# Kernel optimization log

Measured on AMD Instinct MI355X. Metric: run time of the kernel, lower is better.

The kernel has to match this reference:

```python
import jax, jax.numpy as jnp
import numpy as np

NUM_HEADS = 32
NUM_KV_HEADS = 8
HEAD_DIM = 128


def setup_inputs() -> dict:
    key = jax.random.key(0)
    ks = jax.random.split(key, 5)
    B, S, H = 2, 2048, 4096
    Dq = NUM_HEADS * HEAD_DIM      # 4096
    Dkv = NUM_KV_HEADS * HEAD_DIM  # 1024
    return {
        "hidden_states": jax.random.normal(ks[0], (B, S, H), jnp.float32),
        "w_q": jax.random.normal(ks[1], (H, Dq), jnp.float32) * 0.02,
        "w_k": jax.random.normal(ks[2], (H, Dkv), jnp.float32) * 0.02,
        "w_v": jax.random.normal(ks[3], (H, Dkv), jnp.float32) * 0.02,
        "w_o": jax.random.normal(ks[4], (Dq, H), jnp.float32) * 0.02,
    }


def reference(hidden_states, w_q, w_k, w_v, w_o):
    # GQA causal attention, prefill path (no KV cache, RoPE is a no-op in source).
    B, S, _ = hidden_states.shape
    Hq, Hkv, D = NUM_HEADS, NUM_KV_HEADS, HEAD_DIM
    g = Hq // Hkv  # kv groups
    scale = D ** -0.5

    q = (hidden_states @ w_q).reshape(B, S, Hkv, g, D)  # [B,S,Hkv,g,D]
    k = (hidden_states @ w_k).reshape(B, S, Hkv, D)     # [B,S,Hkv,D]
    v = (hidden_states @ w_v).reshape(B, S, Hkv, D)

    # repeat_kv expressed as grouped einsum (avoids materializing repeated K/V)
    scores = jnp.einsum('bqhgd,bkhd->bhgqk', q, k) * scale  # [B,Hkv,g,S,S]
    causal = jnp.tril(jnp.ones((S, S), dtype=bool))
    scores = jnp.where(causal, scores, -jnp.inf)
    probs = jax.nn.softmax(scores.astype(jnp.float32), axis=-1).astype(q.dtype)

    attn = jnp.einsum('bhgqk,bkhd->bqhgd', probs, v)  # [B,S,Hkv,g,D]
    attn = attn.reshape(B, S, Hq * D)
    return attn @ w_o
```

## Files before the change

### kernel.cpp

```cpp
#include <hip/hip_runtime.h>

typedef unsigned short u16;
typedef __attribute__((ext_vector_type(8))) short bf16x8;
typedef __attribute__((ext_vector_type(8))) unsigned short u16x8;
typedef __attribute__((ext_vector_type(4))) unsigned short u16x4;
typedef __attribute__((ext_vector_type(4))) float f32x4;

__device__ __forceinline__ u16 f2bf(float f) {
  union { float f; unsigned u; } v; v.f = f;
  unsigned r = v.u + 0x7fffu + ((v.u >> 16) & 1u);
  return (u16)(r >> 16);
}

__device__ __forceinline__ void gload16(const u16* g, u16* l) {
  __builtin_amdgcn_global_load_lds((const __attribute__((address_space(1))) void*)g,
                                   (__attribute__((address_space(3))) void*)l, 16, 0, 0);
}

__device__ __forceinline__ void transpose_body(const float* __restrict__ in,
                                               u16* __restrict__ out, int K, int N,
                                               int bid, float (*tile)[65]) {
  int nbx = N >> 6;
  int n0 = (bid % nbx) << 6;
  int k0 = (bid / nbx) << 6;
  int tx = threadIdx.x & 15;
  int ty = threadIdx.x >> 4;
#pragma unroll
  for (int r = 0; r < 64; r += 16) {
    float4 v = *(const float4*)(in + (size_t)(k0 + ty + r) * N + n0 + tx * 4);
    tile[ty + r][tx * 4 + 0] = v.x;
    tile[ty + r][tx * 4 + 1] = v.y;
    tile[ty + r][tx * 4 + 2] = v.z;
    tile[ty + r][tx * 4 + 3] = v.w;
  }
  __syncthreads();
#pragma unroll
  for (int r = 0; r < 64; r += 16) {
    u16x4 o;
#pragma unroll
    for (int j = 0; j < 4; j++) o[j] = f2bf(tile[tx * 4 + j][ty + r]);
    *(u16x4*)(out + (size_t)(n0 + ty + r) * K + k0 + tx * 4) = o;
  }
}

__global__ __launch_bounds__(256) void prep_kern(const float* __restrict__ hs,
                                                 const float* __restrict__ wq,
                                                 const float* __restrict__ wk,
                                                 const float* __restrict__ wv,
                                                 const float* __restrict__ wo,
                                                 u16* __restrict__ hs_b,
                                                 u16* __restrict__ wqT,
                                                 u16* __restrict__ wkT,
                                                 u16* __restrict__ wvT,
                                                 u16* __restrict__ woT) {
  __shared__ float tile[64][65];
  int b = blockIdx.x;
  if (b < 8192) {
    int i = (b * 256 + threadIdx.x) * 8;
    float4 a = *(const float4*)(hs + i);
    float4 c = *(const float4*)(hs + i + 4);
    u16x8 r;
    r[0] = f2bf(a.x); r[1] = f2bf(a.y); r[2] = f2bf(a.z); r[3] = f2bf(a.w);
    r[4] = f2bf(c.x); r[5] = f2bf(c.y); r[6] = f2bf(c.z); r[7] = f2bf(c.w);
    *(u16x8*)(hs_b + i) = r;
  } else if (b < 12288) {
    transpose_body(wq, wqT, 4096, 4096, b - 8192, tile);
  } else if (b < 13312) {
    transpose_body(wk, wkT, 4096, 1024, b - 12288, tile);
  } else if (b < 14336) {
    transpose_body(wv, wvT, 4096, 1024, b - 13312, tile);
  } else {
    transpose_body(wo, woT, 4096, 4096, b - 14336, tile);
  }
}

#define PH_PRE()                                           \
  asm volatile("" ::: "memory");                           \
  __builtin_amdgcn_s_barrier();                            \
  asm volatile("" ::: "memory");                           \
  __builtin_amdgcn_s_setprio(1)

#define PH_POST()                                          \
  __builtin_amdgcn_s_setprio(0);                           \
  asm volatile("" ::: "memory");                           \
  __builtin_amdgcn_s_barrier();                            \
  asm volatile("" ::: "memory")

template <int MODE>
__global__ __launch_bounds__(512, 2) void gemm256(const u16* __restrict__ A,
                                                  const u16* __restrict__ Bt,
                                                  void* __restrict__ Cout,
                                                  int M, int N, int K) {
  __shared__ u16 lds[65536];
  const int tid = threadIdx.x;
  const int lane = tid & 63, w = tid >> 6;
  const int wm = w >> 2, wn = w & 3;
  const int li = lane & 15, lg = lane >> 4;
  const int NT = K >> 6;

  const int nbx = N >> 8;
  const int nwg = gridDim.x;
  const int swz = (blockIdx.x & 7) * (nwg >> 3) + (blockIdx.x >> 3);
  const int m0 = (swz / nbx) << 8;
  const int n0 = (swz % nbx) << 8;

  const int srow = w * 16 + (lane >> 3);
  const int scol = ((lane & 7) ^ (lane >> 3)) << 3;
  const u16* sA0 = A + (size_t)(m0 + srow) * K + scol;
  const u16* sA1 = A + (size_t)(m0 + 128 + srow) * K + scol;
  const u16* sB0 = Bt + (size_t)(n0 + srow) * K + scol;
  const u16* sB1 = Bt + (size_t)(n0 + 128 + srow) * K + scol;
  const size_t jK = (size_t)8 * K;
  u16* dA0 = lds + w * 1024;
  u16* dA1 = lds + 8192 + w * 1024;
  u16* dB0 = lds + 32768 + w * 1024;
  u16* dB1 = lds + 32768 + 8192 + w * 1024;

#define STG(sp, dp, t_) do {                                          \
    int db_ = (t_) & 1;                                               \
    gload16((sp) + (size_t)(t_) * 64, (dp) + db_ * 16384);            \
    gload16((sp) + (size_t)(t_) * 64 + jK, (dp) + db_ * 16384 + 512); \
  } while (0)

  STG(sA0, dA0, 0); STG(sA1, dA1, 0); STG(sB0, dB0, 0); STG(sB1, dB1, 0);
  STG(sA0, dA0, 1); STG(sA1, dA1, 1); STG(sB0, dB0, 1); STG(sB1, dB1, 1);
  asm volatile("s_waitcnt vmcnt(8)" ::: "memory");
  __builtin_amdgcn_s_barrier();
  asm volatile("" ::: "memory");

  f32x4 acc[8][4];
#pragma unroll
  for (int m = 0; m < 8; m++)
#pragma unroll
    for (int n = 0; n < 4; n++) acc[m][n] = (f32x4){0.f, 0.f, 0.f, 0.f};

  const int xsw = (li & 7) << 3;
  const int k0o = (lg * 8) ^ xsw;
  const int k1o = (32 + lg * 8) ^ xsw;
  const u16* aBase = lds + wm * 8192;
  const u16* bBase = lds + 32768 + (wn >> 1) * 8192;
  const int brow0 = (wn & 1) * 64;

  bf16x8 a[4][2], b[4][2];

  for (int t = 0; t < NT; ++t) {
    const int db = t & 1;
    const u16* Ab = aBase + db * 16384;
    const u16* Bb = bBase + db * 16384;

#pragma unroll
    for (int mf = 0; mf < 4; mf++) {
      int r = mf * 16 + li;
      a[mf][0] = *(const bf16x8*)(Ab + r * 64 + k0o);
      a[mf][1] = *(const bf16x8*)(Ab + r * 64 + k1o);
    }
#pragma unroll
    for (int nf = 0; nf < 2; nf++) {
      int r = brow0 + nf * 16 + li;
      b[nf][0] = *(const bf16x8*)(Bb + r * 64 + k0o);
      b[nf][1] = *(const bf16x8*)(Bb + r * 64 + k1o);
    }
    PH_PRE();
#pragma unroll
    for (int mf = 0; mf < 4; mf++)
#pragma unroll
      for (int nf = 0; nf < 2; nf++) {
        acc[mf][nf] = __builtin_amdgcn_mfma_f32_16x16x32_bf16(a[mf][0], b[nf][0], acc[mf][nf], 0, 0, 0);
        acc[mf][nf] = __builtin_amdgcn_mfma_f32_16x16x32_bf16(a[mf][1], b[nf][1], acc[mf][nf], 0, 0, 0);
      }
    PH_POST();

#pragma unroll
    for (int nf = 2; nf < 4; nf++) {
      int r = brow0 + nf * 16 + li;
      b[nf][0] = *(const bf16x8*)(Bb + r * 64 + k0o);
      b[nf][1] = *(const bf16x8*)(Bb + r * 64 + k1o);
    }
    PH_PRE();
#pragma unroll
    for (int mf = 0; mf < 4; mf++)
#pragma unroll
      for (int nf = 2; nf < 4; nf++) {
        acc[mf][nf] = __builtin_amdgcn_mfma_f32_16x16x32_bf16(a[mf][0], b[nf][0], acc[mf][nf], 0, 0, 0);
        acc[mf][nf] = __builtin_amdgcn_mfma_f32_16x16x32_bf16(a[mf][1], b[nf][1], acc[mf][nf], 0, 0, 0);
      }
    PH_POST();

#pragma unroll
    for (int mf = 0; mf < 4; mf++) {
      int r = (mf + 4) * 16 + li;
      a[mf][0] = *(const bf16x8*)(Ab + r * 64 + k0o);
      a[mf][1] = *(const bf16x8*)(Ab + r * 64 + k1o);
    }
    if (t + 2 < NT) { STG(sB0, dB0, t + 2); STG(sB1, dB1, t + 2); }
    PH_PRE();
#pragma unroll
    for (int mf = 0; mf < 4; mf++)
#pragma unroll
      for (int nf = 2; nf < 4; nf++) {
        acc[mf + 4][nf] = __builtin_amdgcn_mfma_f32_16x16x32_bf16(a[mf][0], b[nf][0], acc[mf + 4][nf], 0, 0, 0);
        acc[mf + 4][nf] = __builtin_amdgcn_mfma_f32_16x16x32_bf16(a[mf][1], b[nf][1], acc[mf + 4][nf], 0, 0, 0);
      }
    PH_POST();

    if (t + 2 < NT) { STG(sA0, dA0, t + 2); STG(sA1, dA1, t + 2); }
    PH_PRE();
#pragma unroll
    for (int mf = 0; mf < 4; mf++)
#pragma unroll
      for (int nf = 0; nf < 2; nf++) {
        acc[mf + 4][nf] = __builtin_amdgcn_mfma_f32_16x16x32_bf16(a[mf][0], b[nf][0], acc[mf + 4][nf], 0, 0, 0);
        acc[mf + 4][nf] = __builtin_amdgcn_mfma_f32_16x16x32_bf16(a[mf][1], b[nf][1], acc[mf + 4][nf], 0, 0, 0);
      }
    __builtin_amdgcn_s_setprio(0);
    if (t < NT - 2) {
      asm volatile("s_waitcnt vmcnt(8)" ::: "memory");
    } else {
      asm volatile("s_waitcnt vmcnt(0)" ::: "memory");
    }
    __builtin_amdgcn_s_barrier();
    asm volatile("" ::: "memory");
  }

#pragma unroll
  for (int mf = 0; mf < 8; mf++)
#pragma unroll
    for (int nf = 0; nf < 4; nf++)
#pragma unroll
      for (int r = 0; r < 4; r++) {
        int gm = m0 + wm * 128 + mf * 16 + lg * 4 + r;
        int gn = n0 + wn * 64 + nf * 16 + li;
        if (MODE == 0)
          ((u16*)Cout)[(size_t)gm * N + gn] = f2bf(acc[mf][nf][r]);
        else
          ((float*)Cout)[(size_t)gm * N + gn] = acc[mf][nf][r];
      }
#undef STG
}

__global__ __launch_bounds__(512, 2) void gemm_kv(const u16* __restrict__ A,
                                                  const u16* __restrict__ Bt,
                                                  u16* __restrict__ Kout,
                                                  u16* __restrict__ Vout) {
  __shared__ u16 lds[49152];
  const int tid = threadIdx.x;
  const int lane = tid & 63, w = tid >> 6;
  const int wm = w >> 2, wn = w & 3;
  const int li = lane & 15, lg = lane >> 4;
  const int K = 4096, NT = 64;

  const int swz = (blockIdx.x & 7) * 32 + (blockIdx.x >> 3);
  const int m0 = (swz >> 3) << 7;
  const int n0 = (swz & 7) << 8;

  const int srow = w * 16 + (lane >> 3);
  const int scol = ((lane & 7) ^ (lane >> 3)) << 3;
  const u16* sA  = A  + (size_t)(m0 + srow) * K + scol;
  const u16* sB0 = Bt + (size_t)(n0 + srow) * K + scol;
  const u16* sB1 = Bt + (size_t)(n0 + 128 + srow) * K + scol;
  const size_t jK = (size_t)8 * K;
  u16* dA  = lds + w * 1024;
  u16* dB0 = lds + 16384 + w * 1024;
  u16* dB1 = lds + 16384 + 8192 + w * 1024;

#define STGA(t_) do { int db_ = (t_) & 1;                                     \
    gload16(sA + (size_t)(t_) * 64, dA + db_ * 8192);                         \
    gload16(sA + (size_t)(t_) * 64 + jK, dA + db_ * 8192 + 512); } while (0)
#define STGB(t_) do { int db_ = (t_) & 1;                                     \
    gload16(sB0 + (size_t)(t_) * 64, dB0 + db_ * 16384);                      \
    gload16(sB0 + (size_t)(t_) * 64 + jK, dB0 + db_ * 16384 + 512);           \
    gload16(sB1 + (size_t)(t_) * 64, dB1 + db_ * 16384);                      \
    gload16(sB1 + (size_t)(t_) * 64 + jK, dB1 + db_ * 16384 + 512); } while (0)

  STGA(0); STGB(0); STGB(1);
  asm volatile("s_waitcnt vmcnt(4)" ::: "memory");
  __builtin_amdgcn_s_barrier();
  asm volatile("" ::: "memory");

  f32x4 acc[4][4];
#pragma unroll
  for (int m = 0; m < 4; m++)
#pragma unroll
    for (int n = 0; n < 4; n++) acc[m][n] = (f32x4){0.f, 0.f, 0.f, 0.f};

  const int xsw = (li & 7) << 3;
  const int k0o = (lg * 8) ^ xsw;
  const int k1o = (32 + lg * 8) ^ xsw;
  const int arow0 = wm * 64;
  const u16* bBase0 = lds + 16384 + (wn >> 1) * 8192;
  const int brow0 = (wn & 1) * 64;

  bf16x8 a[4][2], b[4][2];

  for (int t = 0; t < NT; ++t) {
    const int db = t & 1;
    const u16* Ab = lds + db * 8192;
    const u16* Bb = bBase0 + db * 16384;

#pragma unroll
    for (int mf = 0; mf < 2; mf++) {
      int r = arow0 + mf * 16 + li;
      a[mf][0] = *(const bf16x8*)(Ab + r * 64 + k0o);
      a[mf][1] = *(const bf16x8*)(Ab + r * 64 + k1o);
    }
#pragma unroll
    for (int nf = 0; nf < 4; nf++) {
      int r = brow0 + nf * 16 + li;
      b[nf][0] = *(const bf16x8*)(Bb + r * 64 + k0o);
      b[nf][1] = *(const bf16x8*)(Bb + r * 64 + k1o);
    }
    if (t + 1 < NT) STGA(t + 1);
    PH_PRE();
#pragma unroll
    for (int mf = 0; mf < 2; mf++)
#pragma unroll
      for (int nf = 0; nf < 4; nf++) {
        acc[mf][nf] = __builtin_amdgcn_mfma_f32_16x16x32_bf16(a[mf][0], b[nf][0], acc[mf][nf], 0, 0, 0);
        acc[mf][nf] = __builtin_amdgcn_mfma_f32_16x16x32_bf16(a[mf][1], b[nf][1], acc[mf][nf], 0, 0, 0);
      }
    PH_POST();

#pragma unroll
    for (int mf = 2; mf < 4; mf++) {
      int r = arow0 + mf * 16 + li;
      a[mf][0] = *(const bf16x8*)(Ab + r * 64 + k0o);
      a[mf][1] = *(const bf16x8*)(Ab + r * 64 + k1o);
    }
    if (t + 2 < NT) STGB(t + 2);
    PH_PRE();
#pragma unroll
    for (int mf = 2; mf < 4; mf++)
#pragma unroll
      for (int nf = 0; nf < 4; nf++) {
        acc[mf][nf] = __builtin_amdgcn_mfma_f32_16x16x32_bf16(a[mf][0], b[nf][0], acc[mf][nf], 0, 0, 0);
        acc[mf][nf] = __builtin_amdgcn_mfma_f32_16x16x32_bf16(a[mf][1], b[nf][1], acc[mf][nf], 0, 0, 0);
      }
    __builtin_amdgcn_s_setprio(0);
    if (t < NT - 2) {
      asm volatile("s_waitcnt vmcnt(4)" ::: "memory");
    } else {
      asm volatile("s_waitcnt vmcnt(0)" ::: "memory");
    }
    __builtin_amdgcn_s_barrier();
    asm volatile("" ::: "memory");
  }

#pragma unroll
  for (int mf = 0; mf < 4; mf++)
#pragma unroll
    for (int nf = 0; nf < 4; nf++)
#pragma unroll
      for (int r = 0; r < 4; r++) {
        int gm = m0 + wm * 64 + mf * 16 + lg * 4 + r;
        int gn = n0 + wn * 64 + nf * 16 + li;
        float val = acc[mf][nf][r];
        if (gn < 1024) {
          Kout[(size_t)gm * 1024 + gn] = f2bf(val);
        } else {
          int c = gn - 1024;
          int b = gm >> 11, s = gm & 2047, kvh = c >> 7, d = c & 127;
          int s2 = (s & ~31) | (((s >> 2) & 3) << 3) | (((s >> 4) & 1) << 2) | (s & 3);
          Vout[(size_t)((b * 8 + kvh) * 128 + d) * 2048 + s2] = f2bf(val);
        }
      }
#undef STGA
#undef STGB
}

__global__ __launch_bounds__(256, 2) void flash_attn_kern(const u16* __restrict__ Qg,
                                                          const u16* __restrict__ Kg,
                                                          const u16* __restrict__ VT,
                                                          u16* __restrict__ Og) {
  const int bid = blockIdx.x;
  const int qt = 63 - (bid >> 4);
  const int gh = bid & 15;
  const int b = gh >> 3, kvh = gh & 7;
  const int tid = threadIdx.x;
  const int lane = tid & 63, w = tid >> 6;
  const int li = lane & 15, lg = lane >> 4;
  const int h = kvh * 4 + w;
  const int q0 = qt << 5;
  const int nt = (qt >> 1) + 1;

  __shared__ u16 Kbuf[2][8192];
  __shared__ u16 Vbuf[2][8192];

  bf16x8 qf[2][4];
  {
    const u16* qp = Qg + ((size_t)(b * 2048 + q0 + li)) * 4096 + h * 128 + lg * 8;
#pragma unroll
    for (int m = 0; m < 2; m++)
#pragma unroll
      for (int ks = 0; ks < 4; ks++)
        qf[m][ks] = *(const bf16x8*)(qp + (size_t)(m * 16) * 4096 + ks * 32);
  }

  const u16* ksrc[4];
  const u16* vsrc[4];
#pragma unroll
  for (int i = 0; i < 4; i++) {
    int c = w * 4 + i;
    int krow = c * 4 + (lane >> 4);
    int kinner = ((lane & 15) * 16) ^ ((krow & 7) << 4);
    ksrc[i] = Kg + (size_t)(b * 2048 + krow) * 1024 + kvh * 128 + (kinner >> 1);
    int vrow = c * 8 + (lane >> 3);
    int vinner = ((lane & 7) * 16) ^ ((vrow & 7) << 4);
    vsrc[i] = VT + (size_t)((b * 8 + kvh) * 128 + vrow) * 2048 + (vinner >> 1);
  }
#pragma unroll
  for (int i = 0; i < 4; i++) {
    int c = w * 4 + i;
    gload16(ksrc[i], &Kbuf[0][c * 512]);
    gload16(vsrc[i], &Vbuf[0][c * 512]);
    ksrc[i] += 64 * 1024;
    vsrc[i] += 64;
  }

  f32x4 oa[2][8];
#pragma unroll
  for (int m = 0; m < 2; m++)
#pragma unroll
    for (int n = 0; n < 8; n++) oa[m][n] = (f32x4){0.f, 0.f, 0.f, 0.f};
  f32x4 lacc[2];
  lacc[0] = (f32x4){0.f, 0.f, 0.f, 0.f};
  lacc[1] = (f32x4){0.f, 0.f, 0.f, 0.f};
  float mrun[2] = {-1e30f, -1e30f};

  const float scale = 0.08838834764831845f;
  bf16x8 onesf;
#pragma unroll
  for (int j = 0; j < 8; j++) onesf[j] = (short)0x3F80;

  asm volatile("s_waitcnt vmcnt(0)\n\ts_barrier" ::: "memory");

  for (int t = 0; t < nt; ++t) {
    const int cur = t & 1;
    const u16* KB = Kbuf[cur];
    const u16* VB = Vbuf[cur];
    if (t + 1 < nt) {
#pragma unroll
      for (int i = 0; i < 4; i++) {
        int c = w * 4 + i;
        gload16(ksrc[i], &Kbuf[cur ^ 1][c * 512]);
        gload16(vsrc[i], &Vbuf[cur ^ 1][c * 512]);
        ksrc[i] += 64 * 1024;
        vsrc[i] += 64;
      }
    }

    f32x4 sacc[2][4];
#pragma unroll
    for (int m = 0; m < 2; m++)
#pragma unroll
      for (int n = 0; n < 4; n++) sacc[m][n] = (f32x4){0.f, 0.f, 0.f, 0.f};
    __builtin_amdgcn_s_setprio(1);
#pragma unroll
    for (int n = 0; n < 4; n++) {
      int krow = n * 16 + li;
      const u16* kb = KB + krow * 128;
      int sw = (krow & 7) << 4;
#pragma unroll
      for (int ks = 0; ks < 4; ks++) {
        bf16x8 kf = *(const bf16x8*)(kb + (((ks * 64 + lg * 16) ^ sw) >> 1));
        sacc[0][n] = __builtin_amdgcn_mfma_f32_16x16x32_bf16(kf, qf[0][ks], sacc[0][n], 0, 0, 0);
        sacc[1][n] = __builtin_amdgcn_mfma_f32_16x16x32_bf16(kf, qf[1][ks], sacc[1][n], 0, 0, 0);
      }
    }
    __builtin_amdgcn_s_setprio(0);

#pragma unroll
    for (int m = 0; m < 2; m++)
#pragma unroll
      for (int n = 0; n < 4; n++)
#pragma unroll
        for (int r = 0; r < 4; r++) sacc[m][n][r] *= scale;
    if (t == nt - 1) {
      const int kv0 = t * 64;
#pragma unroll
      for (int m = 0; m < 2; m++) {
        int q = q0 + m * 16 + li;
#pragma unroll
        for (int n = 0; n < 4; n++)
#pragma unroll
          for (int r = 0; r < 4; r++)
            if (kv0 + n * 16 + lg * 4 + r > q) sacc[m][n][r] = -1e30f;
      }
    }

#pragma unroll
    for (int m = 0; m < 2; m++) {
      float mx = sacc[m][0][0];
#pragma unroll
      for (int n = 0; n < 4; n++)
#pragma unroll
        for (int r = 0; r < 4; r++) mx = fmaxf(mx, sacc[m][n][r]);
      mx = fmaxf(mx, __shfl_xor(mx, 16, 64));
      mx = fmaxf(mx, __shfl_xor(mx, 32, 64));
      float mnew = fmaxf(mrun[m], mx);
      float corr = __expf(mrun[m] - mnew);
      mrun[m] = mnew;
#pragma unroll
      for (int n = 0; n < 4; n++)
#pragma unroll
        for (int r = 0; r < 4; r++) sacc[m][n][r] = __expf(sacc[m][n][r] - mnew);
#pragma unroll
      for (int r = 0; r < 4; r++) lacc[m][r] *= corr;
#pragma unroll
      for (int n = 0; n < 8; n++)
#pragma unroll
        for (int r = 0; r < 4; r++) oa[m][n][r] *= corr;
    }

    bf16x8 pf[2][2];
#pragma unroll
    for (int m = 0; m < 2; m++)
#pragma unroll
      for (int kvs = 0; kvs < 2; kvs++) {
        u16x8 pw;
#pragma unroll
        for (int e = 0; e < 8; e++) pw[e] = f2bf(sacc[m][2 * kvs + (e >> 2)][e & 3]);
        pf[m][kvs] = *(bf16x8*)&pw;
      }

    __builtin_amdgcn_s_setprio(1);
#pragma unroll
    for (int kvs = 0; kvs < 2; kvs++) {
#pragma unroll
      for (int n = 0; n < 8; n++) {
        int vrow = n * 16 + li;
        bf16x8 vf = *(const bf16x8*)(VB + vrow * 64 +
                                     (((kvs * 64 + lg * 16) ^ ((vrow & 7) << 4)) >> 1));
        oa[0][n] = __builtin_amdgcn_mfma_f32_16x16x32_bf16(vf, pf[0][kvs], oa[0][n], 0, 0, 0);
        oa[1][n] = __builtin_amdgcn_mfma_f32_16x16x32_bf16(vf, pf[1][kvs], oa[1][n], 0, 0, 0);
      }
      lacc[0] = __builtin_amdgcn_mfma_f32_16x16x32_bf16(onesf, pf[0][kvs], lacc[0], 0, 0, 0);
      lacc[1] = __builtin_amdgcn_mfma_f32_16x16x32_bf16(onesf, pf[1][kvs], lacc[1], 0, 0, 0);
    }
    __builtin_amdgcn_s_setprio(0);

    asm volatile("s_waitcnt vmcnt(0)\n\ts_barrier" ::: "memory");
  }

#pragma unroll
  for (int m = 0; m < 2; m++) {
    float inv = 1.0f / lacc[m][0];
    u16* op = Og + (size_t)(b * 2048 + q0 + m * 16 + li) * 4096 + h * 128 + lg * 4;
#pragma unroll
    for (int n = 0; n < 8; n++) {
      u16x4 o;
#pragma unroll
      for (int r = 0; r < 4; r++) o[r] = f2bf(oa[m][n][r] * inv);
      *(u16x4*)(op + n * 16) = o;
    }
  }
}

extern "C" void kernel_launch(void* const* d_in, const int* in_sizes, int n_in,
                              void* d_out, int out_size, void* d_ws, size_t ws_size,
                              hipStream_t stream) {
  (void)in_sizes; (void)n_in; (void)out_size; (void)ws_size;
  const float* hs = (const float*)d_in[0];
  const float* wq = (const float*)d_in[1];
  const float* wk = (const float*)d_in[2];
  const float* wv = (const float*)d_in[3];
  const float* wo = (const float*)d_in[4];

  u16* ws   = (u16*)d_ws;
  u16* hs_b = ws;
  u16* wqT  = hs_b + 16777216;
  u16* wkT  = wqT + 16777216;
  u16* wvT  = wkT + 4194304;
  u16* woT  = wvT + 4194304;
  u16* Qb   = woT + 16777216;
  u16* Kb   = Qb + 16777216;
  u16* VTb  = Kb + 4194304;
  u16* attnb = VTb + 4194304;

  prep_kern<<<18432, 256, 0, stream>>>(hs, wq, wk, wv, wo, hs_b, wqT, wkT, wvT, woT);

  gemm256<0><<<256, 512, 0, stream>>>(hs_b, wqT, Qb, 4096, 4096, 4096);
  gemm_kv<<<256, 512, 0, stream>>>(hs_b, wkT, Kb, VTb);

  flash_attn_kern<<<1024, 256, 0, stream>>>(Qb, Kb, VTb, attnb);

  gemm256<2><<<256, 512, 0, stream>>>(attnb, woT, (float*)d_out, 4096, 4096, 4096);
}
```

Measured before the change: 471.4 us.

## Restructure KV GEMM to 256x128 tiles with 4 waves each computing 128x64

The fused K/V projection GEMM moves from 512-thread blocks with 128x256 tiles to 256-thread blocks with 256x128 tiles. Each wave now computes a 128x64 sub-tile with 8x4 accumulators, which doubles MFMA work per LDS fragment load and raises register-level reuse. LDS staging is reorganized to hold four A row-groups and two B row-groups per buffer. The trade-off is higher register pressure and fewer waves per block to hide load latency, and the staging waitcnt counts were left unchanged while loads per stage changed.

```diff
diff --git a/kernel.cpp b/kernel.cpp
--- a/kernel.cpp
+++ b/kernel.cpp
@@ -238,67 +238,77 @@
 #undef STG
 }
 
-__global__ __launch_bounds__(512, 2) void gemm_kv(const u16* __restrict__ A,
+__global__ __launch_bounds__(256, 2) void gemm_kv(const u16* __restrict__ A,
                                                   const u16* __restrict__ Bt,
                                                   u16* __restrict__ Kout,
                                                   u16* __restrict__ Vout) {
   __shared__ u16 lds[49152];
   const int tid = threadIdx.x;
   const int lane = tid & 63, w = tid >> 6;
-  const int wm = w >> 2, wn = w & 3;
+  const int wm = w >> 1, wn = w & 1;
   const int li = lane & 15, lg = lane >> 4;
   const int K = 4096, NT = 64;
 
   const int swz = (blockIdx.x & 7) * 32 + (blockIdx.x >> 3);
-  const int m0 = (swz >> 3) << 7;
-  const int n0 = (swz & 7) << 8;
+  const int m0 = (swz >> 4) << 8;
+  const int n0 = (swz & 15) << 7;
 
   const int srow = w * 16 + (lane >> 3);
   const int scol = ((lane & 7) ^ (lane >> 3)) << 3;
-  const u16* sA  = A  + (size_t)(m0 + srow) * K + scol;
+  const u16* sA0 = A + (size_t)(m0 + srow) * K + scol;
+  const u16* sA1 = A + (size_t)(m0 + 64 + srow) * K + scol;
+  const u16* sA2 = A + (size_t)(m0 + 128 + srow) * K + scol;
+  const u16* sA3 = A + (size_t)(m0 + 192 + srow) * K + scol;
   const u16* sB0 = Bt + (size_t)(n0 + srow) * K + scol;
-  const u16* sB1 = Bt + (size_t)(n0 + 128 + srow) * K + scol;
+  const u16* sB1 = Bt + (size_t)(n0 + 64 + srow) * K + scol;
   const size_t jK = (size_t)8 * K;
-  u16* dA  = lds + w * 1024;
-  u16* dB0 = lds + 16384 + w * 1024;
-  u16* dB1 = lds + 16384 + 8192 + w * 1024;
-
-#define STGA(t_) do { int db_ = (t_) & 1;                                     \
-    gload16(sA + (size_t)(t_) * 64, dA + db_ * 8192);                         \
-    gload16(sA + (size_t)(t_) * 64 + jK, dA + db_ * 8192 + 512); } while (0)
-#define STGB(t_) do { int db_ = (t_) & 1;                                     \
-    gload16(sB0 + (size_t)(t_) * 64, dB0 + db_ * 16384);                      \
-    gload16(sB0 + (size_t)(t_) * 64 + jK, dB0 + db_ * 16384 + 512);           \
-    gload16(sB1 + (size_t)(t_) * 64, dB1 + db_ * 16384);                      \
-    gload16(sB1 + (size_t)(t_) * 64 + jK, dB1 + db_ * 16384 + 512); } while (0)
+  u16* dA0 = lds + w * 1024;
+  u16* dA1 = lds + 4096 + w * 1024;
+  u16* dA2 = lds + 8192 + w * 1024;
+  u16* dA3 = lds + 12288 + w * 1024;
+  u16* dB0 = lds + 32768 + w * 1024;
+  u16* dB1 = lds + 32768 + 4096 + w * 1024;
+
+#define STGH(sp, dp, t_, db_) do {                                    \
+    gload16((sp) + (size_t)(t_) * 64, (dp) + (db_) * 16384);          \
+    gload16((sp) + (size_t)(t_) * 64 + jK, (dp) + (db_) * 16384 + 512); \
+  } while (0)
+#define STGBH(sp, dp, t_, db_) do {                                   \
+    gload16((sp) + (size_t)(t_) * 64, (dp) + (db_) * 8192);           \
+    gload16((sp) + (size_t)(t_) * 64 + jK, (dp) + (db_) * 8192 + 512); \
+  } while (0)
+#define STGA(t_) do { int db_ = (t_) & 1;                             \
+    STGH(sA0, dA0, t_, db_); STGH(sA1, dA1, t_, db_);                 \
+    STGH(sA2, dA2, t_, db_); STGH(sA3, dA3, t_, db_); } while (0)
+#define STGB(t_) do { int db_ = (t_) & 1;                             \
+    STGBH(sB0, dB0, t_, db_); STGBH(sB1, dB1, t_, db_); } while (0)
 
   STGA(0); STGB(0); STGB(1);
   asm volatile("s_waitcnt vmcnt(4)" ::: "memory");
   __builtin_amdgcn_s_barrier();
   asm volatile("" ::: "memory");
 
-  f32x4 acc[4][4];
-#pragma unroll
-  for (int m = 0; m < 4; m++)
+  f32x4 acc[8][4];
+#pragma unroll
+  for (int m = 0; m < 8; m++)
 #pragma unroll
     for (int n = 0; n < 4; n++) acc[m][n] = (f32x4){0.f, 0.f, 0.f, 0.f};
 
   const int xsw = (li & 7) << 3;
   const int k0o = (lg * 8) ^ xsw;
   const int k1o = (32 + lg * 8) ^ xsw;
-  const int arow0 = wm * 64;
-  const u16* bBase0 = lds + 16384 + (wn >> 1) * 8192;
-  const int brow0 = (wn & 1) * 64;
+  const int arow0 = wm * 128;
+  const int brow0 = wn * 64;
 
   bf16x8 a[4][2], b[4][2];
 
   for (int t = 0; t < NT; ++t) {
     const int db = t & 1;
-    const u16* Ab = lds + db * 8192;
-    const u16* Bb = bBase0 + db * 16384;
-
-#pragma unroll
-    for (int mf = 0; mf < 2; mf++) {
+    const u16* Ab = lds + db * 16384;
+    const u16* Bb = lds + 32768 + db * 8192;
+
+#pragma unroll
+    for (int mf = 0; mf < 4; mf++) {
       int r = arow0 + mf * 16 + li;
       a[mf][0] = *(const bf16x8*)(Ab + r * 64 + k0o);
       a[mf][1] = *(const bf16x8*)(Ab + r * 64 + k1o);
@@ -312,7 +322,7 @@
     if (t + 1 < NT) STGA(t + 1);
     PH_PRE();
 #pragma unroll
-    for (int mf = 0; mf < 2; mf++)
+    for (int mf = 0; mf < 4; mf++)
 #pragma unroll
       for (int nf = 0; nf < 4; nf++) {
         acc[mf][nf] = __builtin_amdgcn_mfma_f32_16x16x32_bf16(a[mf][0], b[nf][0], acc[mf][nf], 0, 0, 0);
@@ -321,19 +331,19 @@
     PH_POST();
 
 #pragma unroll
-    for (int mf = 2; mf < 4; mf++) {
-      int r = arow0 + mf * 16 + li;
+    for (int mf = 0; mf < 4; mf++) {
+      int r = arow0 + (mf + 4) * 16 + li;
       a[mf][0] = *(const bf16x8*)(Ab + r * 64 + k0o);
       a[mf][1] = *(const bf16x8*)(Ab + r * 64 + k1o);
     }
     if (t + 2 < NT) STGB(t + 2);
     PH_PRE();
 #pragma unroll
-    for (int mf = 2; mf < 4; mf++)
+    for (int mf = 0; mf < 4; mf++)
 #pragma unroll
       for (int nf = 0; nf < 4; nf++) {
-        acc[mf][nf] = __builtin_amdgcn_mfma_f32_16x16x32_bf16(a[mf][0], b[nf][0], acc[mf][nf], 0, 0, 0);
-        acc[mf][nf] = __builtin_amdgcn_mfma_f32_16x16x32_bf16(a[mf][1], b[nf][1], acc[mf][nf], 0, 0, 0);
+        acc[mf + 4][nf] = __builtin_amdgcn_mfma_f32_16x16x32_bf16(a[mf][0], b[nf][0], acc[mf + 4][nf], 0, 0, 0);
+        acc[mf + 4][nf] = __builtin_amdgcn_mfma_f32_16x16x32_bf16(a[mf][1], b[nf][1], acc[mf + 4][nf], 0, 0, 0);
       }
     __builtin_amdgcn_s_setprio(0);
     if (t < NT - 2) {
@@ -346,12 +356,12 @@
   }
 
 #pragma unroll
-  for (int mf = 0; mf < 4; mf++)
+  for (int mf = 0; mf < 8; mf++)
 #pragma unroll
     for (int nf = 0; nf < 4; nf++)
 #pragma unroll
       for (int r = 0; r < 4; r++) {
-        int gm = m0 + wm * 64 + mf * 16 + lg * 4 + r;
+        int gm = m0 + wm * 128 + mf * 16 + lg * 4 + r;
         int gn = n0 + wn * 64 + nf * 16 + li;
         float val = acc[mf][nf][r];
         if (gn < 1024) {
@@ -363,6 +373,8 @@
           Vout[(size_t)((b * 8 + kvh) * 128 + d) * 2048 + s2] = f2bf(val);
         }
       }
+#undef STGH
+#undef STGBH
 #undef STGA
 #undef STGB
 }
@@ -579,7 +591,7 @@
   prep_kern<<<18432, 256, 0, stream>>>(hs, wq, wk, wv, wo, hs_b, wqT, wkT, wvT, woT);
 
   gemm256<0><<<256, 512, 0, stream>>>(hs_b, wqT, Qb, 4096, 4096, 4096);
-  gemm_kv<<<256, 512, 0, stream>>>(hs_b, wkT, Kb, VTb);
+  gemm_kv<<<256, 256, 0, stream>>>(hs_b, wkT, Kb, VTb);
 
   flash_attn_kern<<<1024, 256, 0, stream>>>(Qb, Kb, VTb, attnb);
 
```

Result: slower. 486.0 us (+3.1%).
